# Optimization experiments

Measured on AMD Instinct MI355X. Metric: run time of the kernel, lower is better.

## Reference

```python
import jax, jax.numpy as jnp
import numpy as np

N_NODES = 100000
N_EDGES = 1600000
N_ADJS = 2
N_LAYERS = 3
D_IN = 128
H = 128           # hidden dim; last conv out = 256 / num_adjs = 128
N_GRAPHS = 1024


def setup_inputs() -> dict:
    key = jax.random.key(0)
    ks = jax.random.split(key, 12)
    x = jax.random.normal(ks[0], (N_NODES, D_IN), dtype=jnp.float32)
    edge_index = jax.random.randint(ks[1], (N_ADJS, 2, N_EDGES), 0, N_NODES, dtype=jnp.int32)
    batch = jnp.sort(jax.random.randint(ks[2], (N_NODES,), 0, N_GRAPHS, dtype=jnp.int32))
    s = 0.05
    lin0_w = jax.random.normal(ks[3], (D_IN, H), dtype=jnp.float32) * s
    lin0_b = jnp.zeros((H,), dtype=jnp.float32)
    conv_w = jax.random.normal(ks[4], (N_ADJS, N_LAYERS, H, H), dtype=jnp.float32) * s
    lin1_w = jax.random.normal(ks[5], (2 * H, H), dtype=jnp.float32) * s
    lin1_b = jnp.zeros((H,), dtype=jnp.float32)
    lin2_w = jax.random.normal(ks[6], (H, 1), dtype=jnp.float32) * s
    lin2_b = jnp.zeros((1,), dtype=jnp.float32)
    return {"x": x, "edge_index": edge_index, "batch": batch,
            "lin0_w": lin0_w, "lin0_b": lin0_b, "conv_w": conv_w,
            "lin1_w": lin1_w, "lin1_b": lin1_b, "lin2_w": lin2_w, "lin2_b": lin2_b}


def _gcn_conv(h, W, row, col, norm, n_nodes):
    # GCNConv (bias=False): out[i] = sum_{j->i} norm_e * (h @ W)[j]
    m = h @ W                                  # [N, H] dense transform first (PyG order)
    msg = m[row] * norm[:, None]               # [E+N, H] gather + edge scaling
    return jax.ops.segment_sum(msg, col, num_segments=n_nodes)


def reference(x, edge_index, batch, lin0_w, lin0_b, conv_w, lin1_w, lin1_b, lin2_w, lin2_b):
    n = x.shape[0]
    loops = jnp.arange(n, dtype=edge_index.dtype)
    x0 = jax.nn.relu(x @ lin0_w + lin0_b)      # lin0 + relu
    pooled = []
    for a in range(N_ADJS):
        # gcn_norm with self loops: deg over targets, norm = d^-1/2[row] * d^-1/2[col]
        row = jnp.concatenate([edge_index[a, 0], loops])
        col = jnp.concatenate([edge_index[a, 1], loops])
        deg = jax.ops.segment_sum(jnp.ones_like(col, dtype=x.dtype), col, num_segments=n)
        dis = jnp.where(deg > 0, jax.lax.rsqrt(jnp.maximum(deg, 1e-12)), 0.0)
        norm = dis[row] * dis[col]
        h = x0
        for l in range(N_LAYERS):
            h = jax.nn.relu(_gcn_conv(h, conv_w[a, l], row, col, norm, n))
        # global_add_pool: segment sum over graph ids
        pooled.append(jax.ops.segment_sum(h, batch, num_segments=N_GRAPHS))
    g = jnp.concatenate(pooled, axis=1)        # [G, 256]
    g = jax.nn.relu(g @ lin1_w + lin1_b)
    # dropout(p=0.5) is identity in eval mode
    return g @ lin2_w + lin2_b                 # [G, 1]
```

## Files before the change

### kernel.cpp

```cpp
#include <hip/hip_runtime.h>

#define NN 100000
#define NE 1600000
#define NADJ 2
#define NLAY 3
#define HD 128
#define NG 1024

#define EB   1563
#define NBUK 391
#define BPAD 400

typedef unsigned int uint32;
typedef unsigned short u16;

typedef __attribute__((ext_vector_type(8))) short bfrag8;
typedef __attribute__((ext_vector_type(4))) float f32x4;
typedef __attribute__((ext_vector_type(2))) float f32x2;

__device__ __forceinline__ u16 f2bf(float f) {
    uint32 u = __float_as_uint(f);
    u += 0x7FFFu + ((u >> 16) & 1u);
    return (u16)(u >> 16);
}
__device__ __forceinline__ float bflo(uint32 u) { return __uint_as_float(u << 16); }
__device__ __forceinline__ float bfhi(uint32 u) { return __uint_as_float(u & 0xFFFF0000u); }

__global__ __launch_bounds__(256) void to_bf16(const float* __restrict__ in,
                                               u16* __restrict__ o) {
    int i = blockIdx.x * 256 + threadIdx.x;
    float4 a = ((const float4*)in)[i * 2];
    float4 b = ((const float4*)in)[i * 2 + 1];
    uint4 v;
    v.x = (uint32)f2bf(a.x) | ((uint32)f2bf(a.y) << 16);
    v.y = (uint32)f2bf(a.z) | ((uint32)f2bf(a.w) << 16);
    v.z = (uint32)f2bf(b.x) | ((uint32)f2bf(b.y) << 16);
    v.w = (uint32)f2bf(b.z) | ((uint32)f2bf(b.w) << 16);
    ((uint4*)o)[i] = v;
}

__global__ void wt_prep(const float* __restrict__ conv_w,
                        const float* __restrict__ lin0_w, u16* __restrict__ wt) {
    const float* W = (blockIdx.x < 6) ? conv_w + (size_t)blockIdx.x * HD * HD
                                      : lin0_w;
    u16* o = wt + (size_t)blockIdx.x * HD * HD;
    for (int i = 0; i < 64; ++i) {
        int idx = i * 256 + threadIdx.x;
        int n = idx >> 7, k = idx & 127;
        o[idx] = f2bf(W[k * 128 + n]);
    }
}

__global__ __launch_bounds__(256) void gemm_mfma(
    const u16* __restrict__ Abf, const u16* __restrict__ Wt,
    u16* __restrict__ outbf, const float* __restrict__ dis,
    const float* __restrict__ bias, int relu)
{
    const int wid = blockIdx.x * 4 + (threadIdx.x >> 6);
    const int lane = threadIdx.x & 63;
    const int row0 = (wid >> 1) * 64;
    if (row0 >= NN) return;
    const int wc = (wid & 1) * 64;
    const int lr = lane & 15, kg = lane >> 4;

    bfrag8 b[4][4];
    #pragma unroll
    for (int ks = 0; ks < 4; ++ks)
        #pragma unroll
        for (int j = 0; j < 4; ++j)
            b[ks][j] = *(const bfrag8*)&Wt[(size_t)(wc + j * 16 + lr) * 128
                                           + (ks * 4 + kg) * 8];

    const f32x4 z = {0.f, 0.f, 0.f, 0.f};
    f32x4 acc[4][4];
    #pragma unroll
    for (int i = 0; i < 4; ++i)
        #pragma unroll
        for (int j = 0; j < 4; ++j) acc[i][j] = z;

    #pragma unroll
    for (int ks = 0; ks < 4; ++ks) {
        bfrag8 a[4];
        #pragma unroll
        for (int i = 0; i < 4; ++i) {
            int r = min(row0 + i * 16 + lr, NN - 1);
            a[i] = *(const bfrag8*)&Abf[(size_t)r * 128 + (ks * 4 + kg) * 8];
        }
        #pragma unroll
        for (int i = 0; i < 4; ++i)
            #pragma unroll
            for (int j = 0; j < 4; ++j)
                acc[i][j] = __builtin_amdgcn_mfma_f32_16x16x32_bf16(
                    a[i], b[ks][j], acc[i][j], 0, 0, 0);
    }

    #pragma unroll
    for (int i = 0; i < 4; ++i) {
        #pragma unroll
        for (int r = 0; r < 4; ++r) {
            int grow = row0 + i * 16 + kg * 4 + r;
            if (grow < NN) {
                float ds = dis ? dis[grow] : 1.f;
                #pragma unroll
                for (int j = 0; j < 4; ++j) {
                    int gcol = wc + j * 16 + lr;
                    float o = acc[i][j][r] * ds;
                    if (bias) o += bias[gcol];
                    if (relu) o = fmaxf(o, 0.f);
                    outbf[(size_t)grow * 128 + gcol] = f2bf(o);
                }
            }
        }
    }
}


__global__ __launch_bounds__(256) void p1_count(
    const int* __restrict__ col, int* __restrict__ bcnt)
{
    __shared__ int h[NBUK];
    int t = threadIdx.x;
    for (int q = t; q < NBUK; q += 256) h[q] = 0;
    __syncthreads();
    int base = blockIdx.x * 1024 + t;
    #pragma unroll
    for (int u = 0; u < 4; ++u) {
        int e = base + u * 256;
        if (e < NE) atomicAdd(&h[col[e] >> 8], 1);
    }
    __syncthreads();
    for (int q = t; q < NBUK; q += 256)
        bcnt[blockIdx.x * BPAD + q] = h[q];
}

__global__ __launch_bounds__(256) void p2a_scanblocks(
    const int* __restrict__ bcnt, int* __restrict__ pscan,
    int* __restrict__ btot)
{
    __shared__ int s[256];
    int b = blockIdx.x;
    int t = threadIdx.x;
    int v[7];
    int loc = 0;
    #pragma unroll
    for (int j = 0; j < 7; ++j) {
        int idx = t * 7 + j;
        v[j] = (idx < EB) ? bcnt[idx * BPAD + b] : 0;
        loc += v[j];
    }
    s[t] = loc;
    __syncthreads();
    for (int off = 1; off < 256; off <<= 1) {
        int u = (t >= off) ? s[t - off] : 0;
        __syncthreads();
        s[t] += u;
        __syncthreads();
    }
    int pre = s[t] - loc;
    #pragma unroll
    for (int j = 0; j < 7; ++j) {
        int idx = t * 7 + j;
        if (idx < EB) pscan[idx * BPAD + b] = pre;
        pre += v[j];
    }
    if (t == 255) btot[b] = s[255];
}

__global__ __launch_bounds__(512) void p2b_scanbuckets(
    const int* __restrict__ btot, int* __restrict__ bbase)
{
    __shared__ int s[512];
    int t = threadIdx.x;
    int v = (t < NBUK) ? btot[t] : 0;
    s[t] = v;
    __syncthreads();
    for (int off = 1; off < 512; off <<= 1) {
        int u = (t >= off) ? s[t - off] : 0;
        __syncthreads();
        s[t] += u;
        __syncthreads();
    }
    if (t < NBUK) bbase[t] = s[t] - v;
    if (t == NBUK - 1) bbase[NBUK] = s[t];
}

__global__ __launch_bounds__(256) void p3_partition(
    const int* __restrict__ row, const int* __restrict__ col,
    const int* __restrict__ pscan, const int* __restrict__ bbase,
    uint2* __restrict__ part)
{
    __shared__ int spre[NBUK];
    __shared__ int cur[NBUK];
    int t = threadIdx.x;
    for (int q = t; q < NBUK; q += 256) {
        spre[q] = bbase[q] + pscan[blockIdx.x * BPAD + q];
        cur[q] = 0;
    }
    __syncthreads();
    int base = blockIdx.x * 1024 + t;
    #pragma unroll
    for (int u = 0; u < 4; ++u) {
        int e = base + u * 256;
        if (e < NE) {
            int c = col[e];
            int b = c >> 8;
            int rk = atomicAdd(&cur[b], 1);
            part[spre[b] + rk] = make_uint2((uint32)row[e], (uint32)c);
        }
    }
}

__global__ __launch_bounds__(256) void p4_csr(
    const uint2* __restrict__ part, const int* __restrict__ bbase,
    int* __restrict__ row_ptr, float* __restrict__ dis,
    int* __restrict__ csr_src)
{
    __shared__ int cnt[256];
    __shared__ int s[256];
    __shared__ int sexcl[256];
    __shared__ int cur[256];
    int b = blockIdx.x, t = threadIdx.x;
    int base = bbase[b];
    int ecnt = bbase[b + 1] - base;
    int n0 = b << 8;
    cnt[t] = 0;
    cur[t] = 0;
    __syncthreads();
    for (int i = t; i < ecnt; i += 256)
        atomicAdd(&cnt[part[base + i].y - n0], 1);
    __syncthreads();
    int v = cnt[t];
    s[t] = v;
    __syncthreads();
    for (int off = 1; off < 256; off <<= 1) {
        int u = (t >= off) ? s[t - off] : 0;
        __syncthreads();
        s[t] += u;
        __syncthreads();
    }
    sexcl[t] = s[t] - v;
    int node = n0 + t;
    if (node < NN) {
        row_ptr[node] = base + s[t] - v;
        dis[node] = rsqrtf((float)(v + 1));
    }
    if (b == 0 && t == 0) row_ptr[NN] = NE;
    __syncthreads();
    for (int i = t; i < ecnt; i += 256) {
        uint2 p = part[base + i];
        int li = (int)p.y - n0;
        int rk = atomicAdd(&cur[li], 1);
        csr_src[base + sexcl[li] + rk] = (int)p.x;
    }
}

__global__ __launch_bounds__(256) void agg_relu(
    const u16* __restrict__ mm, const int* __restrict__ row_ptr,
    const int* __restrict__ csr_src,
    const float* __restrict__ dis, u16* __restrict__ out)
{
    int node = blockIdx.x * 4 + (threadIdx.x >> 6);
    if (node >= NN) return;
    uint32 lane = threadIdx.x & 63;
    const uint32* mv = (const uint32*)mm;
    uint32 self = mv[(uint32)node * 64u + lane];
    f32x2 acc2;
    acc2.x = bflo(self);
    acc2.y = bfhi(self);
    int e0 = row_ptr[node], e1 = row_ptr[node + 1];

    int e = e0;
    for (; e + 16 <= e1; e += 16) {
        uint32 ss[16];
        #pragma unroll
        for (int u = 0; u < 16; ++u) ss[u] = (uint32)csr_src[e + u];
        uint32 vv[16];
        #pragma unroll
        for (int u = 0; u < 16; ++u)
            vv[u] = mv[ss[u] * 64u + lane];
        #pragma unroll
        for (int u = 0; u < 16; ++u) {
            f32x2 tt;
            tt.x = bflo(vv[u]);
            tt.y = bfhi(vv[u]);
            asm("v_pk_add_f32 %0, %0, %1" : "+v"(acc2) : "v"(tt));
        }
    }
    float accx = acc2.x, accy = acc2.y;
    int rem = e1 - e;
    if (rem > 8) {
        uint32 ss[16];
        float mk[16];
        #pragma unroll
        for (int u = 0; u < 16; ++u) {
            int idx = e + u;
            ss[u] = (uint32)csr_src[min(idx, e1 - 1)];
            mk[u] = (idx < e1) ? 1.f : 0.f;
        }
        uint32 vv[16];
        #pragma unroll
        for (int u = 0; u < 16; ++u)
            vv[u] = mv[ss[u] * 64u + lane];
        #pragma unroll
        for (int u = 0; u < 16; ++u) {
            accx = fmaf(mk[u], bflo(vv[u]), accx);
            accy = fmaf(mk[u], bfhi(vv[u]), accy);
        }
    } else if (rem > 0) {
        uint32 ss[8];
        float mk[8];
        #pragma unroll
        for (int u = 0; u < 8; ++u) {
            int idx = e + u;
            ss[u] = (uint32)csr_src[min(idx, e1 - 1)];
            mk[u] = (idx < e1) ? 1.f : 0.f;
        }
        uint32 vv[8];
        #pragma unroll
        for (int u = 0; u < 8; ++u)
            vv[u] = mv[ss[u] * 64u + lane];
        #pragma unroll
        for (int u = 0; u < 8; ++u) {
            accx = fmaf(mk[u], bflo(vv[u]), accx);
            accy = fmaf(mk[u], bfhi(vv[u]), accy);
        }
    }

    float d = dis[node];
    uint32 po = (uint32)f2bf(fmaxf(d * accx, 0.f))
              | ((uint32)f2bf(fmaxf(d * accy, 0.f)) << 16);
    ((uint32*)out)[(uint32)node * 64u + lane] = po;
}

__global__ __launch_bounds__(64) void pool_add(
    const u16* __restrict__ h, const int* __restrict__ batch,
    float* __restrict__ pooled, int aoff)
{
    int c2 = threadIdx.x;
    const uint32* hv = (const uint32*)h;
    int n0 = blockIdx.x * 64;
    int nend = min(n0 + 64, NN);
    int cur = batch[n0];
    float ax = 0.f, ay = 0.f;
    for (int n = n0; n < nend; ++n) {
        int g = batch[n];
        if (g != cur) {
            atomicAdd(&pooled[(size_t)cur * 256 + aoff + 2 * c2], ax);
            atomicAdd(&pooled[(size_t)cur * 256 + aoff + 2 * c2 + 1], ay);
            ax = 0.f; ay = 0.f;
            cur = g;
        }
        uint32 v = hv[(size_t)n * 64 + c2];
        ax += bflo(v);
        ay += bfhi(v);
    }
    atomicAdd(&pooled[(size_t)cur * 256 + aoff + 2 * c2], ax);
    atomicAdd(&pooled[(size_t)cur * 256 + aoff + 2 * c2 + 1], ay);
}

__global__ __launch_bounds__(128) void head(
    const float* __restrict__ pooled,
    const float* __restrict__ w1, const float* __restrict__ b1,
    const float* __restrict__ w2, const float* __restrict__ b2,
    float* __restrict__ out)
{
    __shared__ float sp[256];
    __shared__ float sg[128];
    int g = blockIdx.x, t = threadIdx.x;
    sp[t] = pooled[(size_t)g * 256 + t];
    sp[t + 128] = pooled[(size_t)g * 256 + 128 + t];
    __syncthreads();
    float acc = b1[t];
    #pragma unroll 8
    for (int k = 0; k < 256; ++k) acc = fmaf(sp[k], w1[k * 128 + t], acc);
    sg[t] = fmaxf(acc, 0.f) * w2[t];
    __syncthreads();
    for (int s2 = 64; s2 > 0; s2 >>= 1) {
        if (t < s2) sg[t] += sg[t + s2];
        __syncthreads();
    }
    if (t == 0) out[g] = sg[0] + b2[0];
}

extern "C" void kernel_launch(void* const* d_in, const int* in_sizes, int n_in,
                              void* d_out, int out_size, void* d_ws, size_t ws_size,
                              hipStream_t stream) {
    const float* x      = (const float*)d_in[0];
    const int*   ei     = (const int*)d_in[1];
    const int*   batch  = (const int*)d_in[2];
    const float* lin0_w = (const float*)d_in[3];
    const float* lin0_b = (const float*)d_in[4];
    const float* conv_w = (const float*)d_in[5];
    const float* lin1_w = (const float*)d_in[6];
    const float* lin1_b = (const float*)d_in[7];
    const float* lin2_w = (const float*)d_in[8];
    const float* lin2_b = (const float*)d_in[9];
    float* out = (float*)d_out;

    const size_t NB = (size_t)NN * HD;
    float* x0f    = (float*)d_ws;
    float* bufA   = x0f + NB;
    float* bufB   = bufA + NB;
    float* pooled = bufB + NB;
    int*   row_ptr = (int*)(pooled + (size_t)NG * 256);
    float* dis     = (float*)(row_ptr + NN + 1);
    int*   csr_src = (int*)(dis + NN);
    u16*   wt      = (u16*)(csr_src + NE);
    int*   bcnt    = (int*)(wt + 7 * HD * HD);
    int*   pscan   = bcnt + EB * BPAD;
    int*   btot    = pscan + EB * BPAD;
    int*   bbase   = btot + BPAD;

    u16* x0bf    = (u16*)x0f;
    u16* xbf     = (u16*)(x0f + NB / 2);
    u16* mm      = (u16*)bufA;
    u16* hbuf    = (u16*)bufB;
    uint2* part  = (uint2*)bufA;

    const int GEMM_BLOCKS = (((NN + 63) / 64) * 2 + 3) / 4;

    hipMemsetAsync(pooled, 0, (size_t)NG * 256 * sizeof(float), stream);

    to_bf16<<<NN * HD / 8 / 256, 256, 0, stream>>>(x, xbf);
    wt_prep<<<NADJ * NLAY + 1, 256, 0, stream>>>(conv_w, lin0_w, wt);

    gemm_mfma<<<GEMM_BLOCKS, 256, 0, stream>>>(
        xbf, wt + 6 * HD * HD, x0bf, nullptr, lin0_b, 1);

    for (int a = 0; a < NADJ; ++a) {
        const int* row = ei + (size_t)a * 2 * NE;
        const int* col = row + NE;

        p1_count<<<EB, 256, 0, stream>>>(col, bcnt);
        p2a_scanblocks<<<NBUK, 256, 0, stream>>>(bcnt, pscan, btot);
        p2b_scanbuckets<<<1, 512, 0, stream>>>(btot, bbase);
        p3_partition<<<EB, 256, 0, stream>>>(row, col, pscan, bbase, part);
        p4_csr<<<NBUK, 256, 0, stream>>>(part, bbase, row_ptr, dis, csr_src);

        const u16* h = x0bf;
        for (int l = 0; l < NLAY; ++l) {
            const u16* Wt = wt + ((size_t)a * NLAY + l) * HD * HD;
            gemm_mfma<<<GEMM_BLOCKS, 256, 0, stream>>>(h, Wt, mm, dis,
                                                       nullptr, 0);
            agg_relu<<<(NN + 3) / 4, 256, 0, stream>>>(mm, row_ptr, csr_src,
                                                       dis, hbuf);
            h = hbuf;
        }
        pool_add<<<(NN + 63) / 64, 64, 0, stream>>>(hbuf, batch, pooled, a * HD);
    }

    head<<<NG, 128, 0, stream>>>(pooled, lin1_w, lin1_b, lin2_w, lin2_b, out);
}
```

Baseline: 745.1 us.

## Process two nodes per wavefront in aggregation with readlane-broadcast edge indices

The aggregation kernel now gives each wavefront two adjacent nodes and interleaves their gathers. This is meant to raise memory-level parallelism and hide gather latency. Edge source indices are loaded once per 16 edges into lanes and broadcast with readlane, so they become scalar addresses instead of per-lane redundant loads. The cost is extra code paths for uneven degrees and remainders, and the grid is halved to NN/8 blocks, which relies on NN being divisible by 8.

```diff
diff --git a/kernel.cpp b/kernel.cpp
--- a/kernel.cpp
+++ b/kernel.cpp
@@ -259,77 +259,130 @@
     const int* __restrict__ csr_src,
     const float* __restrict__ dis, u16* __restrict__ out)
 {
-    int node = blockIdx.x * 4 + (threadIdx.x >> 6);
-    if (node >= NN) return;
+    int wid = blockIdx.x * 4 + (threadIdx.x >> 6);
+    int nodeA = wid * 2;
+    if (nodeA >= NN) return;
+    int nodeB = nodeA + 1;
     uint32 lane = threadIdx.x & 63;
     const uint32* mv = (const uint32*)mm;
-    uint32 self = mv[(uint32)node * 64u + lane];
-    f32x2 acc2;
-    acc2.x = bflo(self);
-    acc2.y = bfhi(self);
-    int e0 = row_ptr[node], e1 = row_ptr[node + 1];
-
-    int e = e0;
-    for (; e + 16 <= e1; e += 16) {
-        uint32 ss[16];
-        #pragma unroll
-        for (int u = 0; u < 16; ++u) ss[u] = (uint32)csr_src[e + u];
-        uint32 vv[16];
-        #pragma unroll
-        for (int u = 0; u < 16; ++u)
-            vv[u] = mv[ss[u] * 64u + lane];
+    int lan16 = (int)(lane & 15);
+
+    uint32 selfA = mv[(uint32)nodeA * 64u + lane];
+    uint32 selfB = mv[(uint32)nodeB * 64u + lane];
+    f32x2 accA, accB;
+    accA.x = bflo(selfA); accA.y = bfhi(selfA);
+    accB.x = bflo(selfB); accB.y = bfhi(selfB);
+    int eA = row_ptr[nodeA], e1A = row_ptr[nodeA + 1];
+    int eB = e1A,            e1B = row_ptr[nodeB + 1];
+
+    while (eA + 16 <= e1A && eB + 16 <= e1B) {
+        uint32 pA = (uint32)csr_src[eA + lan16];
+        uint32 pB = (uint32)csr_src[eB + lan16];
         #pragma unroll
         for (int u = 0; u < 16; ++u) {
-            f32x2 tt;
-            tt.x = bflo(vv[u]);
-            tt.y = bfhi(vv[u]);
-            asm("v_pk_add_f32 %0, %0, %1" : "+v"(acc2) : "v"(tt));
-        }
-    }
-    float accx = acc2.x, accy = acc2.y;
-    int rem = e1 - e;
-    if (rem > 8) {
-        uint32 ss[16];
-        float mk[16];
+            uint32 sA = (uint32)__builtin_amdgcn_readlane((int)pA, u);
+            uint32 sB = (uint32)__builtin_amdgcn_readlane((int)pB, u);
+            uint32 vA = (mv + (size_t)sA * 64u)[lane];
+            uint32 vB = (mv + (size_t)sB * 64u)[lane];
+            f32x2 tA, tB;
+            tA.x = bflo(vA); tA.y = bfhi(vA);
+            tB.x = bflo(vB); tB.y = bfhi(vB);
+            asm("v_pk_add_f32 %0, %0, %1" : "+v"(accA) : "v"(tA));
+            asm("v_pk_add_f32 %0, %0, %1" : "+v"(accB) : "v"(tB));
+        }
+        eA += 16; eB += 16;
+    }
+    for (; eA + 16 <= e1A; eA += 16) {
+        uint32 pA = (uint32)csr_src[eA + lan16];
         #pragma unroll
         for (int u = 0; u < 16; ++u) {
-            int idx = e + u;
-            ss[u] = (uint32)csr_src[min(idx, e1 - 1)];
-            mk[u] = (idx < e1) ? 1.f : 0.f;
-        }
-        uint32 vv[16];
-        #pragma unroll
-        for (int u = 0; u < 16; ++u)
-            vv[u] = mv[ss[u] * 64u + lane];
+            uint32 sA = (uint32)__builtin_amdgcn_readlane((int)pA, u);
+            uint32 vA = (mv + (size_t)sA * 64u)[lane];
+            f32x2 tA;
+            tA.x = bflo(vA); tA.y = bfhi(vA);
+            asm("v_pk_add_f32 %0, %0, %1" : "+v"(accA) : "v"(tA));
+        }
+    }
+    for (; eB + 16 <= e1B; eB += 16) {
+        uint32 pB = (uint32)csr_src[eB + lan16];
         #pragma unroll
         for (int u = 0; u < 16; ++u) {
-            accx = fmaf(mk[u], bflo(vv[u]), accx);
-            accy = fmaf(mk[u], bfhi(vv[u]), accy);
-        }
-    } else if (rem > 0) {
-        uint32 ss[8];
-        float mk[8];
-        #pragma unroll
-        for (int u = 0; u < 8; ++u) {
-            int idx = e + u;
-            ss[u] = (uint32)csr_src[min(idx, e1 - 1)];
-            mk[u] = (idx < e1) ? 1.f : 0.f;
-        }
-        uint32 vv[8];
-        #pragma unroll
-        for (int u = 0; u < 8; ++u)
-            vv[u] = mv[ss[u] * 64u + lane];
-        #pragma unroll
-        for (int u = 0; u < 8; ++u) {
-            accx = fmaf(mk[u], bflo(vv[u]), accx);
-            accy = fmaf(mk[u], bfhi(vv[u]), accy);
-        }
-    }
-
-    float d = dis[node];
-    uint32 po = (uint32)f2bf(fmaxf(d * accx, 0.f))
-              | ((uint32)f2bf(fmaxf(d * accy, 0.f)) << 16);
-    ((uint32*)out)[(uint32)node * 64u + lane] = po;
+            uint32 sB = (uint32)__builtin_amdgcn_readlane((int)pB, u);
+            uint32 vB = (mv + (size_t)sB * 64u)[lane];
+            f32x2 tB;
+            tB.x = bflo(vB); tB.y = bfhi(vB);
+            asm("v_pk_add_f32 %0, %0, %1" : "+v"(accB) : "v"(tB));
+        }
+    }
+    int remA = e1A - eA, remB = e1B - eB;
+    if ((remA | remB) != 0) {
+        if (remA > 0 && remB > 0 && remA <= 8 && remB <= 8) {
+            uint32 pA = (uint32)csr_src[min(eA + (int)(lane & 7), e1A - 1)];
+            uint32 pB = (uint32)csr_src[min(eB + (int)(lane & 7), e1B - 1)];
+            #pragma unroll
+            for (int u = 0; u < 8; ++u) {
+                uint32 sA = (uint32)__builtin_amdgcn_readlane((int)pA, u);
+                uint32 sB = (uint32)__builtin_amdgcn_readlane((int)pB, u);
+                uint32 vA = (mv + (size_t)sA * 64u)[lane];
+                uint32 vB = (mv + (size_t)sB * 64u)[lane];
+                float mA = (eA + u < e1A) ? 1.f : 0.f;
+                float mB = (eB + u < e1B) ? 1.f : 0.f;
+                f32x2 tA, tB, kA, kB;
+                tA.x = bflo(vA); tA.y = bfhi(vA); kA.x = mA; kA.y = mA;
+                tB.x = bflo(vB); tB.y = bfhi(vB); kB.x = mB; kB.y = mB;
+                asm("v_pk_fma_f32 %0, %1, %2, %0" : "+v"(accA) : "v"(tA), "v"(kA));
+                asm("v_pk_fma_f32 %0, %1, %2, %0" : "+v"(accB) : "v"(tB), "v"(kB));
+            }
+        } else {
+            uint32 pA = 0, pB = 0;
+            if (remA > 0) pA = (uint32)csr_src[min(eA + lan16, e1A - 1)];
+            if (remB > 0) pB = (uint32)csr_src[min(eB + lan16, e1B - 1)];
+            if (remA > 0 && remB > 0) {
+                #pragma unroll
+                for (int u = 0; u < 16; ++u) {
+                    uint32 sA = (uint32)__builtin_amdgcn_readlane((int)pA, u);
+                    uint32 sB = (uint32)__builtin_amdgcn_readlane((int)pB, u);
+                    uint32 vA = (mv + (size_t)sA * 64u)[lane];
+                    uint32 vB = (mv + (size_t)sB * 64u)[lane];
+                    float mA = (eA + u < e1A) ? 1.f : 0.f;
+                    float mB = (eB + u < e1B) ? 1.f : 0.f;
+                    f32x2 tA, tB, kA, kB;
+                    tA.x = bflo(vA); tA.y = bfhi(vA); kA.x = mA; kA.y = mA;
+                    tB.x = bflo(vB); tB.y = bfhi(vB); kB.x = mB; kB.y = mB;
+                    asm("v_pk_fma_f32 %0, %1, %2, %0" : "+v"(accA) : "v"(tA), "v"(kA));
+                    asm("v_pk_fma_f32 %0, %1, %2, %0" : "+v"(accB) : "v"(tB), "v"(kB));
+                }
+            } else if (remA > 0) {
+                #pragma unroll
+                for (int u = 0; u < 16; ++u) {
+                    uint32 sA = (uint32)__builtin_amdgcn_readlane((int)pA, u);
+                    uint32 vA = (mv + (size_t)sA * 64u)[lane];
+                    float mA = (eA + u < e1A) ? 1.f : 0.f;
+                    f32x2 tA, kA;
+                    tA.x = bflo(vA); tA.y = bfhi(vA); kA.x = mA; kA.y = mA;
+                    asm("v_pk_fma_f32 %0, %1, %2, %0" : "+v"(accA) : "v"(tA), "v"(kA));
+                }
+            } else {
+                #pragma unroll
+                for (int u = 0; u < 16; ++u) {
+                    uint32 sB = (uint32)__builtin_amdgcn_readlane((int)pB, u);
+                    uint32 vB = (mv + (size_t)sB * 64u)[lane];
+                    float mB = (eB + u < e1B) ? 1.f : 0.f;
+                    f32x2 tB, kB;
+                    tB.x = bflo(vB); tB.y = bfhi(vB); kB.x = mB; kB.y = mB;
+                    asm("v_pk_fma_f32 %0, %1, %2, %0" : "+v"(accB) : "v"(tB), "v"(kB));
+                }
+            }
+        }
+    }
+
+    float dA = dis[nodeA], dB = dis[nodeB];
+    uint32 poA = (uint32)f2bf(fmaxf(dA * accA.x, 0.f))
+               | ((uint32)f2bf(fmaxf(dA * accA.y, 0.f)) << 16);
+    uint32 poB = (uint32)f2bf(fmaxf(dB * accB.x, 0.f))
+               | ((uint32)f2bf(fmaxf(dB * accB.y, 0.f)) << 16);
+    ((uint32*)out)[(uint32)nodeA * 64u + lane] = poA;
+    ((uint32*)out)[(uint32)nodeB * 64u + lane] = poB;
 }
 
 __global__ __launch_bounds__(64) void pool_add(
@@ -442,8 +495,8 @@
             const u16* Wt = wt + ((size_t)a * NLAY + l) * HD * HD;
             gemm_mfma<<<GEMM_BLOCKS, 256, 0, stream>>>(h, Wt, mm, dis,
                                                        nullptr, 0);
-            agg_relu<<<(NN + 3) / 4, 256, 0, stream>>>(mm, row_ptr, csr_src,
-                                                       dis, hbuf);
+            agg_relu<<<NN / 8, 256, 0, stream>>>(mm, row_ptr, csr_src,
+                                                 dis, hbuf);
             h = hbuf;
         }
         pool_add<<<(NN + 63) / 64, 64, 0, stream>>>(hbuf, batch, pooled, a * HD);
```

Measured after the change: 733.6 us. Within noise of the previous version (-1.5%).
